# Optimization experiments

Hardware: AMD Instinct MI355X
Metric: run time of the kernel (lower is better)

## Reference

```python
import jax, jax.numpy as jnp
import numpy as np

D = 1024
H = 16
DH = D // H
SCALE = DH ** -0.5
EPS = 1e-5


def setup_inputs() -> dict:
    key = jax.random.key(0)
    ks = jax.random.split(key, 8)
    B, K = 256, 64
    hidden = jax.random.normal(ks[0], (B, K, D), dtype=jnp.float32)
    active_mask = jax.random.bernoulli(ks[1], 0.5, (B, K))
    w = lambda k: jax.random.normal(k, (D, D), dtype=jnp.float32) * 0.02
    return {
        "hidden": hidden,
        "active_mask": active_mask,
        "W_q": w(ks[2]),
        "W_k": w(ks[3]),
        "W_v": w(ks[4]),
        "W_o": w(ks[5]),
        "ln_gamma": jnp.ones((D,), dtype=jnp.float32),
        "ln_beta": jnp.zeros((D,), dtype=jnp.float32),
    }


def reference(hidden, active_mask, W_q, W_k, W_v, W_o, ln_gamma, ln_beta):
    B, K, _ = hidden.shape
    # Linear (no bias): x @ W.T, then split heads -> [B, H, K, Dh]
    def heads(t):
        return t.reshape(B, K, H, DH).transpose(0, 2, 1, 3)
    Q = heads(hidden @ W_q.T)
    Km = heads(hidden @ W_k.T)
    V = heads(hidden @ W_v.T)
    # scaled dot-product scores [B, H, K, K]
    attn = jnp.einsum("bhqd,bhkd->bhqk", Q, Km) * SCALE
    attn = jax.nn.softmax(attn, axis=-1)
    # post-softmax row masking: inactive query rows get zero attention
    row_mask = active_mask[:, None, :, None].astype(attn.dtype)  # [B,1,K,1]
    attn = attn * row_mask
    out = jnp.einsum("bhqk,bhkd->bhqd", attn, V)
    out = out.transpose(0, 2, 1, 3).reshape(B, K, D)
    out = out @ W_o.T
    # gated residual: residual attention output only on active modules
    active_f = active_mask[:, :, None].astype(hidden.dtype)
    h_final = hidden + active_f * out
    # LayerNorm over last dim
    mu = jnp.mean(h_final, axis=-1, keepdims=True)
    var = jnp.var(h_final, axis=-1, keepdims=True)
    h_norm = (h_final - mu) * jax.lax.rsqrt(var + EPS)
    return h_norm * ln_gamma + ln_beta
```

## Files before the change

### kernel.cpp

```cpp
#include <hip/hip_runtime.h>
#include <hip/hip_bf16.h>
#include <stdint.h>

#define D_DIM 1024
#define NH 16
#define DHD 64
#define SEQ 64
#define NBATCH 256
#define M_TOT 16384
#define ATT_SCALE 0.125f
#define LN_EPS 1e-5f

#define BM 256
#define BN 256
#define BKT 64
#define NTK (D_DIM / BKT)

typedef __attribute__((ext_vector_type(8))) short bf16x8;
typedef __attribute__((ext_vector_type(4))) float f32x4;

__device__ __forceinline__ float bf2f(short s) {
  union { uint32_t u; float f; } c;
  c.u = ((uint32_t)(uint16_t)s) << 16;
  return c.f;
}

__device__ __forceinline__ short f2bf(float f) {
  union { __hip_bfloat16 h; short s; } c; c.h = __float2bfloat16(f);
  return c.s;
}

__device__ __forceinline__ bf16x8 cvt8(float4 a, float4 b) {
  bf16x8 r;
  r[0] = f2bf(a.x); r[1] = f2bf(a.y); r[2] = f2bf(a.z); r[3] = f2bf(a.w);
  r[4] = f2bf(b.x); r[5] = f2bf(b.y); r[6] = f2bf(b.z); r[7] = f2bf(b.w);
  return r;
}

__device__ __forceinline__ void cp16(const void* g, void* l) {
  __builtin_amdgcn_global_load_lds(
      (const __attribute__((address_space(1))) uint32_t*)g,
      (__attribute__((address_space(3))) uint32_t*)l, 16, 0, 0);
}

__global__ void conv_all(const float* __restrict__ Wq, const float* __restrict__ Wk,
                         const float* __restrict__ Wv, const float* __restrict__ Wo,
                         const float* __restrict__ H,
                         __hip_bfloat16* __restrict__ Wall,
                         __hip_bfloat16* __restrict__ Hb) {
  const size_t idx8 = ((size_t)blockIdx.x * 256 + threadIdx.x) * 8;
  const size_t WE = (size_t)4 * D_DIM * D_DIM;
  const float* src;
  __hip_bfloat16* dst;
  if (idx8 < WE) {
    int z = (int)(idx8 >> 20);
    size_t off = idx8 & ((1u << 20) - 1);
    src = ((z == 0) ? Wq : (z == 1) ? Wk : (z == 2) ? Wv : Wo) + off;
    dst = Wall + idx8;
  } else {
    size_t off = idx8 - WE;
    src = H + off;
    dst = Hb + off;
  }
  float4 a = ((const float4*)src)[0];
  float4 b = ((const float4*)src)[1];
  *(bf16x8*)(short*)dst = cvt8(a, b);
}

#define GEMM_TILE(J, CUR, NXT) do {                                           \
                          \
    _Pragma("unroll") for (int q_ = 0; q_ < 2; ++q_) {                        \
      bl[q_][0] = *(const bf16x8*)(LdsB[CUR] + boff + q_ * 2048 + colsw0);    \
      bl[q_][1] = *(const bf16x8*)(LdsB[CUR] + boff + q_ * 2048 + colsw1);    \
    }                                                                         \
    _Pragma("unroll") for (int q_ = 0; q_ < 2; ++q_) {                        \
      bh[q_][0] =                                                             \
          *(const bf16x8*)(LdsB[CUR] + boff + (2 + q_) * 2048 + colsw0);      \
      bh[q_][1] =                                                             \
          *(const bf16x8*)(LdsB[CUR] + boff + (2 + q_) * 2048 + colsw1);      \
    }                                                                         \
    _Pragma("unroll") for (int i_ = 0; i_ < 4; ++i_) {                        \
      ah[i_][0] =                                                             \
          *(const bf16x8*)(LdsA[CUR] + aoff + 8192 + i_ * 2048 + colsw0);     \
      ah[i_][1] =                                                             \
          *(const bf16x8*)(LdsA[CUR] + aoff + 8192 + i_ * 2048 + colsw1);     \
    }                                                                         \
    __builtin_amdgcn_s_setprio(1);                                            \
    _Pragma("unroll") for (int i_ = 0; i_ < 4; ++i_)                          \
      _Pragma("unroll") for (int q_ = 0; q_ < 2; ++q_) {                      \
        acc[i_][q_] = __builtin_amdgcn_mfma_f32_16x16x32_bf16(                \
            al[i_][0], bl[q_][0], acc[i_][q_], 0, 0, 0);                      \
        acc[i_][q_] = __builtin_amdgcn_mfma_f32_16x16x32_bf16(                \
            al[i_][1], bl[q_][1], acc[i_][q_], 0, 0, 0);                      \
      }                                                                       \
    _Pragma("unroll") for (int i_ = 0; i_ < 4; ++i_)                          \
      _Pragma("unroll") for (int q_ = 0; q_ < 2; ++q_) {                      \
        acc[i_][2 + q_] = __builtin_amdgcn_mfma_f32_16x16x32_bf16(            \
            al[i_][0], bh[q_][0], acc[i_][2 + q_], 0, 0, 0);                  \
        acc[i_][2 + q_] = __builtin_amdgcn_mfma_f32_16x16x32_bf16(            \
            al[i_][1], bh[q_][1], acc[i_][2 + q_], 0, 0, 0);                  \
      }                                                                       \
    _Pragma("unroll") for (int i_ = 0; i_ < 4; ++i_)                          \
      _Pragma("unroll") for (int q_ = 0; q_ < 2; ++q_) {                      \
        acc[4 + i_][2 + q_] = __builtin_amdgcn_mfma_f32_16x16x32_bf16(        \
            ah[i_][0], bh[q_][0], acc[4 + i_][2 + q_], 0, 0, 0);              \
        acc[4 + i_][2 + q_] = __builtin_amdgcn_mfma_f32_16x16x32_bf16(        \
            ah[i_][1], bh[q_][1], acc[4 + i_][2 + q_], 0, 0, 0);              \
      }                                                                       \
    __builtin_amdgcn_s_setprio(0);                                            \
    __asm volatile("s_waitcnt lgkmcnt(0)" ::: "memory");                      \
    __builtin_amdgcn_sched_barrier(0);                                        \
    __builtin_amdgcn_s_barrier();                                             \
               \
    if ((J) + 2 < NTK) {                                                      \
      STG_A(CUR, (J) + 2, 0); STG_A(CUR, (J) + 2, 1);                         \
      STG_A(CUR, (J) + 2, 2); STG_A(CUR, (J) + 2, 3);                         \
      STG_B(CUR, (J) + 2, 0); STG_B(CUR, (J) + 2, 1);                         \
      STG_B(CUR, (J) + 2, 2); STG_B(CUR, (J) + 2, 3);                         \
      __asm volatile("s_waitcnt vmcnt(8)" ::: "memory");                      \
    } else if ((J) + 1 < NTK) {                                               \
      __asm volatile("s_waitcnt vmcnt(0)" ::: "memory");                      \
    }                                                                         \
    if ((J) + 1 < NTK) {                                                      \
      __builtin_amdgcn_s_barrier();                                           \
      _Pragma("unroll") for (int i_ = 0; i_ < 4; ++i_) {                      \
        al[i_][0] = *(const bf16x8*)(LdsA[NXT] + aoff + i_ * 2048 + colsw0);  \
        al[i_][1] = *(const bf16x8*)(LdsA[NXT] + aoff + i_ * 2048 + colsw1);  \
      }                                                                       \
    }                                                                         \
    __builtin_amdgcn_s_setprio(1);                                            \
    _Pragma("unroll") for (int i_ = 0; i_ < 4; ++i_)                          \
      _Pragma("unroll") for (int q_ = 0; q_ < 2; ++q_) {                      \
        acc[4 + i_][q_] = __builtin_amdgcn_mfma_f32_16x16x32_bf16(            \
            ah[i_][0], bl[q_][0], acc[4 + i_][q_], 0, 0, 0);                  \
        acc[4 + i_][q_] = __builtin_amdgcn_mfma_f32_16x16x32_bf16(            \
            ah[i_][1], bl[q_][1], acc[4 + i_][q_], 0, 0, 0);                  \
      }                                                                       \
    __builtin_amdgcn_s_setprio(0);                                            \
  } while (0)

#define GEMM_PIPELINE() do {                                                  \
         \
    STG_A(0, 0, 0); STG_A(0, 0, 1); STG_A(0, 0, 2); STG_A(0, 0, 3);           \
    STG_B(0, 0, 0); STG_B(0, 0, 1); STG_B(0, 0, 2); STG_B(0, 0, 3);           \
    STG_A(1, 1, 0); STG_A(1, 1, 1); STG_A(1, 1, 2); STG_A(1, 1, 3);           \
    STG_B(1, 1, 0); STG_B(1, 1, 1); STG_B(1, 1, 2); STG_B(1, 1, 3);           \
    __asm volatile("s_waitcnt vmcnt(8)" ::: "memory");                        \
    __builtin_amdgcn_s_barrier();                                             \
    _Pragma("unroll") for (int i_ = 0; i_ < 4; ++i_) {                        \
      al[i_][0] = *(const bf16x8*)(LdsA[0] + aoff + i_ * 2048 + colsw0);      \
      al[i_][1] = *(const bf16x8*)(LdsA[0] + aoff + i_ * 2048 + colsw1);      \
    }                                                                         \
    _Pragma("unroll 1") for (int it_ = 0; it_ < NTK / 2; ++it_) {             \
      GEMM_TILE(2 * it_, 0, 1);                                               \
      GEMM_TILE(2 * it_ + 1, 1, 0);                                           \
    }                                                                         \
  } while (0)

__global__ void __launch_bounds__(512, 2)
gemm_qkv_bf(const __hip_bfloat16* __restrict__ Hb,
            const __hip_bfloat16* __restrict__ Wall,
            __hip_bfloat16* __restrict__ Qw,
            __hip_bfloat16* __restrict__ Kw,
            __hip_bfloat16* __restrict__ Vtw) {
  __shared__ __align__(16) char LdsA[2][BM * BKT * 2];
  __shared__ __align__(16) char LdsB[2][BN * BKT * 2];
  const int tid = threadIdx.x;
  const int lane = tid & 63, wave = tid >> 6;
  const int l16 = lane & 15, kq = lane >> 4;
  const int wr = wave >> 2, wc = wave & 3;
  const int m0 = blockIdx.x * BM, n0 = blockIdx.y * BN;
  const __hip_bfloat16* Bm = Wall + (size_t)blockIdx.z * D_DIM * D_DIM;
  const int wub = wave * 1024;
  const int srow = tid >> 3;
  const int scol8 = (((tid >> 3) & 7) ^ (tid & 7)) << 3;
  const size_t a_thr = (size_t)(m0 + srow) * D_DIM + scol8;
  const size_t b_thr = (size_t)(n0 + srow) * D_DIM + scol8;
  const int colsw0 = (kq * 16) ^ ((l16 & 7) << 4);
  const int colsw1 = (64 + kq * 16) ^ ((l16 & 7) << 4);
  const int aoff = (wr * 128 + l16) * 128;
  const int boff = (wc * 64 + l16) * 128;

  f32x4 acc[8][4] = {};
  bf16x8 al[4][2], ah[4][2], bl[2][2], bh[2][2];

#define STG_A(BUF, JT, Q)                                                      \
  cp16(Hb + a_thr + (size_t)(Q) * (64 * D_DIM) + (JT) * BKT,                   \
       LdsA[BUF] + (Q) * 8192 + wub)
#define STG_B(BUF, JT, Q)                                                      \
  cp16(Bm + b_thr + (size_t)(Q) * (64 * D_DIM) + (JT) * BKT,                   \
       LdsB[BUF] + (Q) * 8192 + wub)

  GEMM_PIPELINE();

#undef STG_A
#undef STG_B

  __hip_bfloat16* outp = (blockIdx.z == 0) ? Qw : (blockIdx.z == 1) ? Kw : Vtw;
  const int zlt2 = (blockIdx.z < 2);
#pragma unroll
  for (int i = 0; i < 8; ++i) {
#pragma unroll
    for (int r = 0; r < 4; ++r) {
      int gm = m0 + wr * 128 + i * 16 + kq * 4 + r;
      int b = gm >> 6, ks = gm & 63;
#pragma unroll
      for (int jf = 0; jf < 4; ++jf) {
        int gn = n0 + wc * 64 + jf * 16 + l16;
        int h = gn >> 6, dh = gn & 63;
        size_t idx = zlt2 ? ((size_t)(b * NH + h) * SEQ + ks) * DHD + dh
                          : ((size_t)(b * NH + h) * DHD + dh) * SEQ + ks;
        outp[idx] = __float2bfloat16(acc[i][jf][r]);
      }
    }
  }
}

__global__ void attn_v2(__hip_bfloat16* Qw,
                        const __hip_bfloat16* __restrict__ Kw,
                        const __hip_bfloat16* __restrict__ Vtw,
                        const int* __restrict__ mask) {
  __shared__ __align__(16) __hip_bfloat16 Ps[4][16 * 72];
  const int tid = threadIdx.x;
  const int lane = tid & 63;
  const int wave = tid >> 6;
  const int l16 = lane & 15, kq = lane >> 4;
  const int hh = blockIdx.x * 4 + wave;
  const int b = hh >> 4;
  const size_t base = (size_t)hh * 4096;
  __hip_bfloat16* Pw = &Ps[wave][0];

  bf16x8 kf[2][4], vf[2][4], qf[4][2];
#pragma unroll
  for (int kk2 = 0; kk2 < 2; ++kk2)
#pragma unroll
    for (int j = 0; j < 4; ++j) {
      kf[kk2][j] = *(const bf16x8*)(Kw + base + (j * 16 + l16) * 64 + kk2 * 32 + kq * 8);
      vf[kk2][j] = *(const bf16x8*)(Vtw + base + (j * 16 + l16) * 64 + kk2 * 32 + kq * 8);
    }
#pragma unroll
  for (int qt = 0; qt < 4; ++qt)
#pragma unroll
    for (int kk2 = 0; kk2 < 2; ++kk2)
      qf[qt][kk2] = *(const bf16x8*)(Qw + base + (qt * 16 + l16) * 64 + kk2 * 32 + kq * 8);

#pragma unroll
  for (int qt = 0; qt < 4; ++qt) {
    f32x4 accS[4] = {};
#pragma unroll
    for (int kk2 = 0; kk2 < 2; ++kk2)
#pragma unroll
      for (int j = 0; j < 4; ++j)
        accS[j] = __builtin_amdgcn_mfma_f32_16x16x32_bf16(qf[qt][kk2], kf[kk2][j],
                                                          accS[j], 0, 0, 0);
#pragma unroll
    for (int r = 0; r < 4; ++r) {
      float sv[4];
      float m = -1e30f;
#pragma unroll
      for (int j = 0; j < 4; ++j) { sv[j] = accS[j][r] * ATT_SCALE; m = fmaxf(m, sv[j]); }
#pragma unroll
      for (int off = 1; off < 16; off <<= 1) m = fmaxf(m, __shfl_xor(m, off, 64));
      float s = 0.f;
#pragma unroll
      for (int j = 0; j < 4; ++j) { sv[j] = __expf(sv[j] - m); s += sv[j]; }
#pragma unroll
      for (int off = 1; off < 16; off <<= 1) s += __shfl_xor(s, off, 64);
      float inv = 1.0f / s;
      int ql = kq * 4 + r;
#pragma unroll
      for (int j = 0; j < 4; ++j)
        Pw[ql * 72 + j * 16 + l16] = __float2bfloat16(sv[j] * inv);
    }
    __asm volatile("s_waitcnt lgkmcnt(0)" ::: "memory");

    f32x4 accO[4] = {};
#pragma unroll
    for (int kk2 = 0; kk2 < 2; ++kk2) {
      bf16x8 a = *(const bf16x8*)((const short*)Pw + l16 * 72 + kk2 * 32 + kq * 8);
#pragma unroll
      for (int j = 0; j < 4; ++j)
        accO[j] = __builtin_amdgcn_mfma_f32_16x16x32_bf16(a, vf[kk2][j], accO[j], 0, 0, 0);
    }
    __asm volatile("s_waitcnt lgkmcnt(0)" ::: "memory");

#pragma unroll
    for (int r = 0; r < 4; ++r) {
      int q = qt * 16 + kq * 4 + r;
      float mk = mask[b * SEQ + q] ? 1.0f : 0.0f;
#pragma unroll
      for (int j = 0; j < 4; ++j)
        Qw[base + q * DHD + j * 16 + l16] = __float2bfloat16(accO[j][r] * mk);
    }
  }
}

__global__ void __launch_bounds__(512, 2)
gemm_o(const __hip_bfloat16* __restrict__ Ow,
       const __hip_bfloat16* __restrict__ WoB,
       const int* __restrict__ mask,
       __hip_bfloat16* Hb) {
  __shared__ __align__(16) char LdsA[2][BM * BKT * 2];
  __shared__ __align__(16) char LdsB[2][BN * BKT * 2];
  const int tid = threadIdx.x;
  const int lane = tid & 63, wave = tid >> 6;
  const int l16 = lane & 15, kq = lane >> 4;
  const int wr = wave >> 2, wc = wave & 3;
  const int m0 = blockIdx.x * BM, n0 = blockIdx.y * BN;
  const int wub = wave * 1024;
  const int srow = tid >> 3;
  const int scol8 = (((tid >> 3) & 7) ^ (tid & 7)) << 3;
  const size_t ao_thr = ((size_t)(m0 >> 6) << 16) + (srow << 6) + scol8;
  const size_t b_thr = (size_t)(n0 + srow) * D_DIM + scol8;
  const int colsw0 = (kq * 16) ^ ((l16 & 7) << 4);
  const int colsw1 = (64 + kq * 16) ^ ((l16 & 7) << 4);
  const int aoff = (wr * 128 + l16) * 128;
  const int boff = (wc * 64 + l16) * 128;

  f32x4 acc[8][4] = {};
  bf16x8 al[4][2], ah[4][2], bl[2][2], bh[2][2];

#define STG_A(BUF, JT, Q)                                                      \
  cp16(Ow + ao_thr + ((size_t)(Q) << 16) + ((size_t)(JT) << 12),               \
       LdsA[BUF] + (Q) * 8192 + wub)
#define STG_B(BUF, JT, Q)                                                      \
  cp16(WoB + b_thr + (size_t)(Q) * (64 * D_DIM) + (JT) * BKT,                  \
       LdsB[BUF] + (Q) * 8192 + wub)

  GEMM_PIPELINE();

#undef STG_A
#undef STG_B

#pragma unroll
  for (int i = 0; i < 8; ++i) {
#pragma unroll
    for (int r = 0; r < 4; ++r) {
      int gm = m0 + wr * 128 + i * 16 + kq * 4 + r;
      float mk = mask[gm] ? 1.0f : 0.0f;
#pragma unroll
      for (int jf = 0; jf < 4; ++jf) {
        int gn = n0 + wc * 64 + jf * 16 + l16;
        size_t idx = (size_t)gm * D_DIM + gn;
        Hb[idx] = __float2bfloat16(__bfloat162float(Hb[idx]) + mk * acc[i][jf][r]);
      }
    }
  }
}

__global__ void ln_bf(const __hip_bfloat16* __restrict__ Hf,
                      const float* __restrict__ gamma,
                      const float* __restrict__ beta,
                      float* __restrict__ out) {
  __shared__ float red[4];
  const int row = blockIdx.x, tid = threadIdx.x;
  const int wave = tid >> 6, lane = tid & 63;
  const size_t boff = (size_t)row * D_DIM + tid * 8;

  bf16x8 v = *(const bf16x8*)((const short*)Hf + boff);
  float f[8], s = 0.f, ss = 0.f;
#pragma unroll
  for (int k = 0; k < 8; ++k) { f[k] = bf2f(v[k]); s += f[k]; ss += f[k] * f[k]; }
#pragma unroll
  for (int off = 1; off < 64; off <<= 1) {
    s += __shfl_xor(s, off, 64);
    ss += __shfl_xor(ss, off, 64);
  }
  if (lane == 0) { red[wave * 2] = s; red[wave * 2 + 1] = ss; }
  __syncthreads();
  s = red[0] + red[2];
  ss = red[1] + red[3];
  const float mu = s * (1.0f / D_DIM);
  const float var = ss * (1.0f / D_DIM) - mu * mu;
  const float rs = rsqrtf(var + LN_EPS);

  float4 g0 = ((const float4*)(gamma + tid * 8))[0];
  float4 g1 = ((const float4*)(gamma + tid * 8))[1];
  float4 b0 = ((const float4*)(beta + tid * 8))[0];
  float4 b1 = ((const float4*)(beta + tid * 8))[1];
  float g[8] = {g0.x, g0.y, g0.z, g0.w, g1.x, g1.y, g1.z, g1.w};
  float bb[8] = {b0.x, b0.y, b0.z, b0.w, b1.x, b1.y, b1.z, b1.w};
  float o[8];
#pragma unroll
  for (int k = 0; k < 8; ++k)
    o[k] = (f[k] - mu) * rs * g[k] + bb[k];
  ((float4*)(out + boff))[0] = make_float4(o[0], o[1], o[2], o[3]);
  ((float4*)(out + boff))[1] = make_float4(o[4], o[5], o[6], o[7]);
}

extern "C" void kernel_launch(void* const* d_in, const int* in_sizes, int n_in,
                              void* d_out, int out_size, void* d_ws, size_t ws_size,
                              hipStream_t stream) {
  const float* hidden = (const float*)d_in[0];
  const int* mask = (const int*)d_in[1];
  const float* Wq = (const float*)d_in[2];
  const float* Wk = (const float*)d_in[3];
  const float* Wv = (const float*)d_in[4];
  const float* Wo = (const float*)d_in[5];
  const float* gamma = (const float*)d_in[6];
  const float* beta = (const float*)d_in[7];
  float* out = (float*)d_out;

  const size_t SZ = (size_t)M_TOT * D_DIM;
  __hip_bfloat16* Hb   = (__hip_bfloat16*)d_ws;
  __hip_bfloat16* Kw   = Hb + SZ;
  __hip_bfloat16* Qw   = Hb + 2 * SZ;
  __hip_bfloat16* Vtw  = Hb + 3 * SZ;
  __hip_bfloat16* Wall = Hb + 4 * SZ;

  conv_all<<<dim3(10240), 256, 0, stream>>>(Wq, Wk, Wv, Wo, hidden, Wall, Hb);
  gemm_qkv_bf<<<dim3(64, 4, 3), 512, 0, stream>>>(Hb, Wall, Qw, Kw, Vtw);
  attn_v2<<<dim3(1024), 256, 0, stream>>>(Qw, Kw, Vtw, mask);
  gemm_o<<<dim3(64, 4), 512, 0, stream>>>(Qw, Wall + 3 * D_DIM * D_DIM, mask, Hb);
  ln_bf<<<dim3(16384), 128, 0, stream>>>(Hb, gamma, beta, out);
}
```

Before: 339.8 us.

## Load GEMM B operand directly from global memory into registers, dropping LDS staging

The QKV and output-projection GEMMs no longer stage the weight (B) tile through shared memory. Each wave now reads its B fragments straight from global memory into registers every k-step, while the A tile is still double-buffered in LDS. The aim is to halve LDS footprint and LDS traffic, which may allow more occupancy. The cost is that the B loads are no longer prefetched ahead of use. They are also duplicated across waves sharing columns, and the tile loop is restructured with an extra barrier, exposing global latency inside the MFMA loop.

```diff
diff --git a/kernel.cpp b/kernel.cpp
--- a/kernel.cpp
+++ b/kernel.cpp
@@ -67,93 +67,57 @@
   *(bf16x8*)(short*)dst = cvt8(a, b);
 }
 
-#define GEMM_TILE(J, CUR, NXT) do {                                           \
-                          \
-    _Pragma("unroll") for (int q_ = 0; q_ < 2; ++q_) {                        \
-      bl[q_][0] = *(const bf16x8*)(LdsB[CUR] + boff + q_ * 2048 + colsw0);    \
-      bl[q_][1] = *(const bf16x8*)(LdsB[CUR] + boff + q_ * 2048 + colsw1);    \
-    }                                                                         \
-    _Pragma("unroll") for (int q_ = 0; q_ < 2; ++q_) {                        \
-      bh[q_][0] =                                                             \
-          *(const bf16x8*)(LdsB[CUR] + boff + (2 + q_) * 2048 + colsw0);      \
-      bh[q_][1] =                                                             \
-          *(const bf16x8*)(LdsB[CUR] + boff + (2 + q_) * 2048 + colsw1);      \
-    }                                                                         \
+#define GEMM_TILE(J, CUR) do {                                                \
+    _Pragma("unroll") for (int q_ = 0; q_ < 4; ++q_)                          \
+      _Pragma("unroll") for (int k2 = 0; k2 < 2; ++k2)                        \
+        bq[q_][k2] = *(const bf16x8*)(bbase + (size_t)q_ * (16 * D_DIM) +     \
+                                      (J) * BKT + k2 * 32);                   \
     _Pragma("unroll") for (int i_ = 0; i_ < 4; ++i_) {                        \
+      al[i_][0] = *(const bf16x8*)(LdsA[CUR] + aoff + i_ * 2048 + colsw0);    \
+      al[i_][1] = *(const bf16x8*)(LdsA[CUR] + aoff + i_ * 2048 + colsw1);    \
       ah[i_][0] =                                                             \
           *(const bf16x8*)(LdsA[CUR] + aoff + 8192 + i_ * 2048 + colsw0);     \
       ah[i_][1] =                                                             \
           *(const bf16x8*)(LdsA[CUR] + aoff + 8192 + i_ * 2048 + colsw1);     \
     }                                                                         \
-    __builtin_amdgcn_s_setprio(1);                                            \
-    _Pragma("unroll") for (int i_ = 0; i_ < 4; ++i_)                          \
-      _Pragma("unroll") for (int q_ = 0; q_ < 2; ++q_) {                      \
-        acc[i_][q_] = __builtin_amdgcn_mfma_f32_16x16x32_bf16(                \
-            al[i_][0], bl[q_][0], acc[i_][q_], 0, 0, 0);                      \
-        acc[i_][q_] = __builtin_amdgcn_mfma_f32_16x16x32_bf16(                \
-            al[i_][1], bl[q_][1], acc[i_][q_], 0, 0, 0);                      \
-      }                                                                       \
-    _Pragma("unroll") for (int i_ = 0; i_ < 4; ++i_)                          \
-      _Pragma("unroll") for (int q_ = 0; q_ < 2; ++q_) {                      \
-        acc[i_][2 + q_] = __builtin_amdgcn_mfma_f32_16x16x32_bf16(            \
-            al[i_][0], bh[q_][0], acc[i_][2 + q_], 0, 0, 0);                  \
-        acc[i_][2 + q_] = __builtin_amdgcn_mfma_f32_16x16x32_bf16(            \
-            al[i_][1], bh[q_][1], acc[i_][2 + q_], 0, 0, 0);                  \
-      }                                                                       \
-    _Pragma("unroll") for (int i_ = 0; i_ < 4; ++i_)                          \
-      _Pragma("unroll") for (int q_ = 0; q_ < 2; ++q_) {                      \
-        acc[4 + i_][2 + q_] = __builtin_amdgcn_mfma_f32_16x16x32_bf16(        \
-            ah[i_][0], bh[q_][0], acc[4 + i_][2 + q_], 0, 0, 0);              \
-        acc[4 + i_][2 + q_] = __builtin_amdgcn_mfma_f32_16x16x32_bf16(        \
-            ah[i_][1], bh[q_][1], acc[4 + i_][2 + q_], 0, 0, 0);              \
-      }                                                                       \
-    __builtin_amdgcn_s_setprio(0);                                            \
     __asm volatile("s_waitcnt lgkmcnt(0)" ::: "memory");                      \
     __builtin_amdgcn_sched_barrier(0);                                        \
     __builtin_amdgcn_s_barrier();                                             \
-               \
     if ((J) + 2 < NTK) {                                                      \
       STG_A(CUR, (J) + 2, 0); STG_A(CUR, (J) + 2, 1);                         \
       STG_A(CUR, (J) + 2, 2); STG_A(CUR, (J) + 2, 3);                         \
-      STG_B(CUR, (J) + 2, 0); STG_B(CUR, (J) + 2, 1);                         \
-      STG_B(CUR, (J) + 2, 2); STG_B(CUR, (J) + 2, 3);                         \
-      __asm volatile("s_waitcnt vmcnt(8)" ::: "memory");                      \
-    } else if ((J) + 1 < NTK) {                                               \
+      __asm volatile("s_waitcnt vmcnt(4)" ::: "memory");                      \
+    } else {                                                                  \
       __asm volatile("s_waitcnt vmcnt(0)" ::: "memory");                      \
-    }                                                                         \
-    if ((J) + 1 < NTK) {                                                      \
-      __builtin_amdgcn_s_barrier();                                           \
-      _Pragma("unroll") for (int i_ = 0; i_ < 4; ++i_) {                      \
-        al[i_][0] = *(const bf16x8*)(LdsA[NXT] + aoff + i_ * 2048 + colsw0);  \
-        al[i_][1] = *(const bf16x8*)(LdsA[NXT] + aoff + i_ * 2048 + colsw1);  \
-      }                                                                       \
     }                                                                         \
     __builtin_amdgcn_s_setprio(1);                                            \
     _Pragma("unroll") for (int i_ = 0; i_ < 4; ++i_)                          \
-      _Pragma("unroll") for (int q_ = 0; q_ < 2; ++q_) {                      \
+      _Pragma("unroll") for (int q_ = 0; q_ < 4; ++q_) {                      \
+        acc[i_][q_] = __builtin_amdgcn_mfma_f32_16x16x32_bf16(                \
+            al[i_][0], bq[q_][0], acc[i_][q_], 0, 0, 0);                      \
+        acc[i_][q_] = __builtin_amdgcn_mfma_f32_16x16x32_bf16(                \
+            al[i_][1], bq[q_][1], acc[i_][q_], 0, 0, 0);                      \
+      }                                                                       \
+    _Pragma("unroll") for (int i_ = 0; i_ < 4; ++i_)                          \
+      _Pragma("unroll") for (int q_ = 0; q_ < 4; ++q_) {                      \
         acc[4 + i_][q_] = __builtin_amdgcn_mfma_f32_16x16x32_bf16(            \
-            ah[i_][0], bl[q_][0], acc[4 + i_][q_], 0, 0, 0);                  \
+            ah[i_][0], bq[q_][0], acc[4 + i_][q_], 0, 0, 0);                  \
         acc[4 + i_][q_] = __builtin_amdgcn_mfma_f32_16x16x32_bf16(            \
-            ah[i_][1], bl[q_][1], acc[4 + i_][q_], 0, 0, 0);                  \
+            ah[i_][1], bq[q_][1], acc[4 + i_][q_], 0, 0, 0);                  \
       }                                                                       \
     __builtin_amdgcn_s_setprio(0);                                            \
+    __builtin_amdgcn_s_barrier();                                             \
   } while (0)
 
 #define GEMM_PIPELINE() do {                                                  \
-         \
+                          \
     STG_A(0, 0, 0); STG_A(0, 0, 1); STG_A(0, 0, 2); STG_A(0, 0, 3);           \
-    STG_B(0, 0, 0); STG_B(0, 0, 1); STG_B(0, 0, 2); STG_B(0, 0, 3);           \
     STG_A(1, 1, 0); STG_A(1, 1, 1); STG_A(1, 1, 2); STG_A(1, 1, 3);           \
-    STG_B(1, 1, 0); STG_B(1, 1, 1); STG_B(1, 1, 2); STG_B(1, 1, 3);           \
-    __asm volatile("s_waitcnt vmcnt(8)" ::: "memory");                        \
+    __asm volatile("s_waitcnt vmcnt(4)" ::: "memory");                        \
     __builtin_amdgcn_s_barrier();                                             \
-    _Pragma("unroll") for (int i_ = 0; i_ < 4; ++i_) {                        \
-      al[i_][0] = *(const bf16x8*)(LdsA[0] + aoff + i_ * 2048 + colsw0);      \
-      al[i_][1] = *(const bf16x8*)(LdsA[0] + aoff + i_ * 2048 + colsw1);      \
-    }                                                                         \
     _Pragma("unroll 1") for (int it_ = 0; it_ < NTK / 2; ++it_) {             \
-      GEMM_TILE(2 * it_, 0, 1);                                               \
-      GEMM_TILE(2 * it_ + 1, 1, 0);                                           \
+      GEMM_TILE(2 * it_, 0);                                                  \
+      GEMM_TILE(2 * it_ + 1, 1);                                              \
     }                                                                         \
   } while (0)
 
@@ -164,7 +128,6 @@
             __hip_bfloat16* __restrict__ Kw,
             __hip_bfloat16* __restrict__ Vtw) {
   __shared__ __align__(16) char LdsA[2][BM * BKT * 2];
-  __shared__ __align__(16) char LdsB[2][BN * BKT * 2];
   const int tid = threadIdx.x;
   const int lane = tid & 63, wave = tid >> 6;
   const int l16 = lane & 15, kq = lane >> 4;
@@ -175,26 +138,22 @@
   const int srow = tid >> 3;
   const int scol8 = (((tid >> 3) & 7) ^ (tid & 7)) << 3;
   const size_t a_thr = (size_t)(m0 + srow) * D_DIM + scol8;
-  const size_t b_thr = (size_t)(n0 + srow) * D_DIM + scol8;
+  const __hip_bfloat16* bbase =
+      Bm + (size_t)(n0 + wc * 64 + l16) * D_DIM + kq * 8;
   const int colsw0 = (kq * 16) ^ ((l16 & 7) << 4);
   const int colsw1 = (64 + kq * 16) ^ ((l16 & 7) << 4);
   const int aoff = (wr * 128 + l16) * 128;
-  const int boff = (wc * 64 + l16) * 128;
 
   f32x4 acc[8][4] = {};
-  bf16x8 al[4][2], ah[4][2], bl[2][2], bh[2][2];
+  bf16x8 al[4][2], ah[4][2], bq[4][2];
 
 #define STG_A(BUF, JT, Q)                                                      \
   cp16(Hb + a_thr + (size_t)(Q) * (64 * D_DIM) + (JT) * BKT,                   \
        LdsA[BUF] + (Q) * 8192 + wub)
-#define STG_B(BUF, JT, Q)                                                      \
-  cp16(Bm + b_thr + (size_t)(Q) * (64 * D_DIM) + (JT) * BKT,                   \
-       LdsB[BUF] + (Q) * 8192 + wub)
 
   GEMM_PIPELINE();
 
 #undef STG_A
-#undef STG_B
 
   __hip_bfloat16* outp = (blockIdx.z == 0) ? Qw : (blockIdx.z == 1) ? Kw : Vtw;
   const int zlt2 = (blockIdx.z < 2);
@@ -301,7 +260,6 @@
        const int* __restrict__ mask,
        __hip_bfloat16* Hb) {
   __shared__ __align__(16) char LdsA[2][BM * BKT * 2];
-  __shared__ __align__(16) char LdsB[2][BN * BKT * 2];
   const int tid = threadIdx.x;
   const int lane = tid & 63, wave = tid >> 6;
   const int l16 = lane & 15, kq = lane >> 4;
@@ -311,26 +269,22 @@
   const int srow = tid >> 3;
   const int scol8 = (((tid >> 3) & 7) ^ (tid & 7)) << 3;
   const size_t ao_thr = ((size_t)(m0 >> 6) << 16) + (srow << 6) + scol8;
-  const size_t b_thr = (size_t)(n0 + srow) * D_DIM + scol8;
+  const __hip_bfloat16* bbase =
+      WoB + (size_t)(n0 + wc * 64 + l16) * D_DIM + kq * 8;
   const int colsw0 = (kq * 16) ^ ((l16 & 7) << 4);
   const int colsw1 = (64 + kq * 16) ^ ((l16 & 7) << 4);
   const int aoff = (wr * 128 + l16) * 128;
-  const int boff = (wc * 64 + l16) * 128;
 
   f32x4 acc[8][4] = {};
-  bf16x8 al[4][2], ah[4][2], bl[2][2], bh[2][2];
+  bf16x8 al[4][2], ah[4][2], bq[4][2];
 
 #define STG_A(BUF, JT, Q)                                                      \
   cp16(Ow + ao_thr + ((size_t)(Q) << 16) + ((size_t)(JT) << 12),               \
        LdsA[BUF] + (Q) * 8192 + wub)
-#define STG_B(BUF, JT, Q)                                                      \
-  cp16(WoB + b_thr + (size_t)(Q) * (64 * D_DIM) + (JT) * BKT,                  \
-       LdsB[BUF] + (Q) * 8192 + wub)
 
   GEMM_PIPELINE();
 
 #undef STG_A
-#undef STG_B
 
 #pragma unroll
   for (int i = 0; i < 8; ++i) {
```

New measurement: 425.9 us. 1.25x slower.
